# Kernel tuning notes

Measured on AMD Instinct MI355X. Metric: run time of the kernel, lower is better.

## Reference

```python
import jax, jax.numpy as jnp
import numpy as np

N, E, G = 20000, 320000, 256      # nodes, edges, graphs per batch
IN, D, P = 128, 256, 16           # input_dim, out_dim, n_prot
EPS, R, TEMP = 1e-7, 0.5, 0.2


def setup_inputs() -> dict:
    key = jax.random.key(0)
    ks = jax.random.split(key, 9)
    x = jax.random.normal(ks[0], (N, IN), jnp.float32)
    edge_index = jax.random.randint(ks[1], (2, E), 0, N)
    batch = jnp.sort(jax.random.randint(ks[2], (N,), 0, G))
    def w(k, sh):
        fan_in = sh[0]
        return jax.random.normal(k, sh, jnp.float32) * (1.0 / fan_in) ** 0.5
    return {
        "x": x, "edge_index": edge_index, "batch": batch,
        "W1": w(ks[3], (IN, D)), "b1": jnp.zeros((D,), jnp.float32),
        "W2": w(ks[4], (D, D)), "b2": jnp.zeros((D,), jnp.float32),
        "Wm1": w(ks[5], (2 * D, D)), "bm1": jnp.zeros((D,), jnp.float32),
        "Wm2": w(ks[6], (D, 1)), "bm2": jnp.zeros((1,), jnp.float32),
        "prototypes": jax.random.normal(ks[7], (P, D), jnp.float32),
    }


def _cosine(a, b):
    # prototype_distances: cosine similarity with zero-norm -> eps fixup (eval path, no softmax)
    na = jnp.linalg.norm(a, axis=1)
    na = jnp.where(na == 0, na + EPS, na)
    nb = jnp.linalg.norm(b, axis=1)
    nb = jnp.where(nb == 0, nb + EPS, nb)
    return jnp.einsum('ik,jk->ij', a, b) / (na[:, None] * nb[None, :])


def _encoder(x, src, dst, batch, W1, b1, W2, b2, atten=None):
    # 2-layer GIN: h' = relu((h + sum_{j->i} atten_ji * h_j) W + b); graph emb = sum pool
    def conv(h, W, b):
        msg = h[src]                                   # [E, d]
        if atten is not None:
            msg = msg * atten                          # [E, 1] broadcast
        agg = h + jax.ops.segment_sum(msg, dst, num_segments=N)
        return jax.nn.relu(agg @ W + b)
    h = conv(x, W1, b1)
    h = conv(h, W2, b2)
    g = jax.ops.segment_sum(h, batch, num_segments=G)  # [G, D]
    return g, h


def reference(x, edge_index, batch, W1, b1, W2, b2, Wm1, bm1, Wm2, bm2, prototypes):
    src, dst = edge_index[0], edge_index[1]
    graph_embs, node_embs = _encoder(x, src, dst, batch, W1, b1, W2, b2)

    # eval path: assign each graph to nearest prototype by cosine similarity
    sim0 = _cosine(graph_embs, prototypes)             # [G, P]
    assign_prot = jnp.argmax(sim0, axis=1)             # [G]

    # sample_subgraph (eval: plain sigmoid, no gumbel noise)
    node_proto = prototypes[assign_prot[batch]]        # [N, D]
    h = jnp.concatenate([node_embs, node_proto], axis=-1)
    node_prob = jax.nn.relu(h @ Wm1 + bm1) @ Wm2 + bm2  # [N, 1]
    node_bern = jax.nn.sigmoid(node_prob)              # [N, 1]
    edge_bern = node_bern[src] * node_bern[dst]        # [E, 1]

    x2 = x * node_bern
    subgraph_embs, _ = _encoder(x2, src, dst, batch, W1, b1, W2, b2, atten=edge_bern)

    similarity = _cosine(subgraph_embs, prototypes)    # [G, P]

    # NCE loss
    a2 = jnp.argmax(similarity, axis=1)
    onehot = jax.nn.one_hot(a2, P, dtype=similarity.dtype)
    se = jnp.exp(similarity / TEMP)
    pos = (se * onehot).sum(axis=1)
    neg = (se * (1.0 - onehot)).sum(axis=1)
    NCE_loss = -jnp.log(pos / neg).mean()

    # KL regularizers
    nb = node_bern
    KL_node = (nb * jnp.log(nb / R + EPS)
               + (1 - nb) * jnp.log((1 - nb) / (1 - R + EPS) + EPS)).mean()
    eb = edge_bern
    KL_edge = (eb * jnp.log(eb / (R * R) + EPS)
               + (1 - eb) * jnp.log((1 - eb) / (1 - R * R + EPS) + EPS)).mean()
    KL_loss = KL_node + KL_edge

    data_sim = _cosine(subgraph_embs, subgraph_embs)   # [G, G]
    return (KL_loss, NCE_loss, similarity, node_bern, edge_bern,
            data_sim, subgraph_embs, node_embs)
```

## Files before the change

kernel.cpp:

```cpp
#include <hip/hip_runtime.h>
#include <cmath>
#include <cstdint>

#define DINL __device__ __forceinline__

namespace {

constexpr int Nn = 20000, Ee = 320000, Gg = 256, Dd = 256, Pp = 16;
constexpr int Npad = 20096;
constexpr float EPSf = 1e-7f, Rf = 0.5f, TEMPf = 0.2f;

typedef unsigned short u16;
typedef __attribute__((ext_vector_type(8))) short short8;
typedef __attribute__((ext_vector_type(4))) float floatx4;
typedef __attribute__((ext_vector_type(2))) unsigned int u2v;
typedef __attribute__((ext_vector_type(4))) unsigned int u4v;

DINL float waveSum(float x) {
#pragma unroll
  for (int off = 32; off > 0; off >>= 1) x += __shfl_xor(x, off, 64);
  return x;
}

DINL u16 f2bf(float f) {
  unsigned u = __float_as_uint(f);
  unsigned r = u + 0x7fffu + ((u >> 16) & 1u);
  return (u16)(r >> 16);
}
DINL float bf2f(u16 h) { return __uint_as_float(((unsigned)h) << 16); }

__global__ void k_deg(const int* __restrict__ dst, int* __restrict__ deg) {
  int e = blockIdx.x * 256 + threadIdx.x;
  if (e < Ee) atomicAdd(&deg[dst[e]], 1);
}

__global__ __launch_bounds__(1024) void k_pre(const int* __restrict__ deg,
                                              int* __restrict__ offs,
                                              const int* __restrict__ batch,
                                              int* __restrict__ goff) {
  int tid = threadIdx.x;
  if (blockIdx.x == 0) {
    __shared__ int part[1024];
    const int chunk = (Nn + 1023) >> 10;
    int start = tid * chunk;
    int s = 0;
    for (int k = 0; k < chunk; k++) { int i = start + k; if (i < Nn) s += deg[i]; }
    part[tid] = s;
    __syncthreads();
    for (int off = 1; off < 1024; off <<= 1) {
      int v = (tid >= off) ? part[tid - off] : 0;
      __syncthreads();
      part[tid] += v;
      __syncthreads();
    }
    int run = (tid == 0) ? 0 : part[tid - 1];
    for (int k = 0; k < chunk; k++) {
      int i = start + k;
      if (i < Nn) { offs[i] = run; run += deg[i]; }
    }
    if (start < Nn && start + chunk >= Nn) offs[Nn] = run;
  } else {
    for (int i = tid; i < Nn; i += 1024) {
      int bi = batch[i];
      int bp = (i == 0) ? -1 : batch[i - 1];
      for (int g = bp + 1; g <= bi; ++g) goff[g] = i;
      if (i == Nn - 1)
        for (int g = bi + 1; g <= Gg; ++g) goff[g] = Nn;
    }
  }
}

__global__ void k_fill(const int* __restrict__ src, const int* __restrict__ dst,
                       const int* __restrict__ offs, int* __restrict__ cursor,
                       int* __restrict__ csr) {
  int e = blockIdx.x * 256 + threadIdx.x;
  if (e < Ee) {
    int d = dst[e];
    int pos = atomicAdd(&cursor[d], 1);
    csr[offs[d] + pos] = src[e];
  }
}

template <int DIM, int EPL, bool INBF>
DINL void slice(float r[EPL], const void* __restrict__ hv, int row, int ce) {
  if constexpr (INBF) {
    const u16* p = (const u16*)hv + (size_t)row * DIM + ce;
    ushort4 u = *(const ushort4*)p;
    r[0] = bf2f(u.x); r[1] = bf2f(u.y); r[2] = bf2f(u.z); r[3] = bf2f(u.w);
  } else {
    const float* p = (const float*)hv + (size_t)row * DIM + ce;
    float2 u = *(const float2*)p;
    r[0] = u.x; r[1] = u.y;
  }
}

template <int DIM, int MODE, bool INBF, bool OSPL>
__global__ __launch_bounds__(256) void k_aggc(
    const void* __restrict__ hv, const float* __restrict__ nb,
    const int* __restrict__ offs, const int* __restrict__ csr,
    u16* __restrict__ oh, u16* __restrict__ ol) {
  constexpr int EPL = INBF ? 4 : 2;
  constexpr int COLS = EPL * 16;
  constexpr int CHUNKS = DIM / COLS;
  int c = (int)(blockIdx.x % CHUNKS);
  int grp = (int)(blockIdx.x / CHUNKS);
  int wv = threadIdx.x >> 6, lane = threadIdx.x & 63;
  int sub = lane >> 4, l = lane & 15;
  int node = grp * 16 + wv * 4 + sub;
  if (node >= Nn) return;
  int ce = c * COLS + l * EPL;
  float self[EPL], ts[EPL];
  slice<DIM, EPL, INBF>(self, hv, node, ce);
#pragma unroll
  for (int j = 0; j < EPL; j++) ts[j] = 0.f;
  int beg = offs[node], end = offs[node + 1];
  int k = beg;
  for (; k + 4 <= end; k += 4) {
    int s0 = csr[k], s1 = csr[k + 1], s2 = csr[k + 2], s3 = csr[k + 3];
    float r0[EPL], r1[EPL], r2[EPL], r3[EPL];
    slice<DIM, EPL, INBF>(r0, hv, s0, ce);
    slice<DIM, EPL, INBF>(r1, hv, s1, ce);
    slice<DIM, EPL, INBF>(r2, hv, s2, ce);
    slice<DIM, EPL, INBF>(r3, hv, s3, ce);
    if (MODE == 0) {
#pragma unroll
      for (int j = 0; j < EPL; j++) ts[j] += (r0[j] + r1[j]) + (r2[j] + r3[j]);
    } else {
      float w0 = nb[s0], w1 = nb[s1], w2 = nb[s2], w3 = nb[s3];
      if (MODE == 1) { w0 *= w0; w1 *= w1; w2 *= w2; w3 *= w3; }
#pragma unroll
      for (int j = 0; j < EPL; j++)
        ts[j] += (w0 * r0[j] + w1 * r1[j]) + (w2 * r2[j] + w3 * r3[j]);
    }
  }
  for (; k < end; k++) {
    int s = csr[k];
    float r[EPL];
    slice<DIM, EPL, INBF>(r, hv, s, ce);
    if (MODE == 0) {
#pragma unroll
      for (int j = 0; j < EPL; j++) ts[j] += r[j];
    } else {
      float wq = nb[s];
      if (MODE == 1) wq *= wq;
#pragma unroll
      for (int j = 0; j < EPL; j++) ts[j] += wq * r[j];
    }
  }
  float val[EPL];
  if (MODE == 0) {
#pragma unroll
    for (int j = 0; j < EPL; j++) val[j] = self[j] + ts[j];
  } else if (MODE == 1) {
    float wi = nb[node];
#pragma unroll
    for (int j = 0; j < EPL; j++) val[j] = wi * (self[j] + ts[j]);
  } else {
    float wi = nb[node];
#pragma unroll
    for (int j = 0; j < EPL; j++) val[j] = self[j] + wi * ts[j];
  }
  u16 hs[EPL], ls[EPL];
#pragma unroll
  for (int j = 0; j < EPL; j++) {
    hs[j] = f2bf(val[j]);
    if (OSPL) ls[j] = f2bf(val[j] - bf2f(hs[j]));
  }
  u16* po = oh + (size_t)node * DIM + ce;
  if constexpr (EPL == 2) {
    unsigned v = (unsigned)hs[0] | ((unsigned)hs[1] << 16);
    __builtin_nontemporal_store(v, (unsigned*)po);
  } else {
    u2v v;
    v.x = (unsigned)hs[0] | ((unsigned)hs[1] << 16);
    v.y = (unsigned)hs[2] | ((unsigned)hs[3] << 16);
    __builtin_nontemporal_store(v, (u2v*)po);
  }
  if constexpr (OSPL) {
    u16* pl = ol + (size_t)node * DIM + ce;
    if constexpr (EPL == 2) {
      unsigned v = (unsigned)ls[0] | ((unsigned)ls[1] << 16);
      __builtin_nontemporal_store(v, (unsigned*)pl);
    } else {
      u2v v;
      v.x = (unsigned)ls[0] | ((unsigned)ls[1] << 16);
      v.y = (unsigned)ls[2] | ((unsigned)ls[3] << 16);
      __builtin_nontemporal_store(v, (u2v*)pl);
    }
  }
}

template <int K, bool SPLIT, int MODE>
__global__ __launch_bounds__(256) void k_mm(
    const u16* __restrict__ Ah, const u16* __restrict__ Al,
    const u16* __restrict__ Bh, const u16* __restrict__ Bl,
    const float* __restrict__ bias,
    float* __restrict__ outF, u16* __restrict__ outH, u16* __restrict__ outL,
    const float* __restrict__ pc, const int* __restrict__ batch,
    const int* __restrict__ assign, const float* __restrict__ Wm2,
    float* __restrict__ prob) {
  int b = (int)blockIdx.x;
  int g = b >> 5, lane5 = b & 31;
  int panel = g * 8 + (lane5 & 7);
  int col = lane5 >> 3;
  if (panel >= 157) return;
  int rowBase = panel * 128, colBase = col * 64;

  constexpr int SK = 40;
  __shared__ u16 AsH[128 * SK];
  __shared__ u16 AsL[SPLIT ? 128 * SK : 16];
  __shared__ u16 BsH[64 * SK];
  __shared__ u16 BsL[SPLIT ? 64 * SK : 16];
  __shared__ int ap_s[128];
  int t = threadIdx.x;
  if (MODE == 1 && t < 128) {
    int r = rowBase + t;
    ap_s[t] = (r < Nn) ? assign[batch[r]] : 0;
  }
  int lane = t & 63, wv = t >> 6;
  int quad = lane >> 4, l16 = lane & 15;
  int wm = wv * 32;
  floatx4 acc[2][4];
#pragma unroll
  for (int mt = 0; mt < 2; mt++)
#pragma unroll
    for (int nt = 0; nt < 4; nt++) acc[mt][nt] = (floatx4){0.f, 0.f, 0.f, 0.f};

  int ar = t >> 1;
  int ak = (t & 1) * 16;
  const u16* agH = Ah + (size_t)(rowBase + ar) * K + ak;
  const u16* agL = Al + (size_t)(rowBase + ar) * K + ak;
  int bn = t >> 2;
  int bk = (t & 3) * 8;
  const u16* bgH = Bh + (size_t)(colBase + bn) * K + bk;
  const u16* bgL = Bl + (size_t)(colBase + bn) * K + bk;

  u4v cA0 = *(const u4v*)(agH);
  u4v cA1 = *(const u4v*)(agH + 8);
  u4v cB0 = *(const u4v*)(bgH);
  u4v cA0l, cA1l, cB0l;
  if constexpr (SPLIT) {
    cA0l = *(const u4v*)(agL);
    cA1l = *(const u4v*)(agL + 8);
    cB0l = *(const u4v*)(bgL);
  }

  for (int k0 = 0; k0 < K; k0 += 32) {
    __syncthreads();
    *(u4v*)&AsH[ar * SK + ak] = cA0;
    *(u4v*)&AsH[ar * SK + ak + 8] = cA1;
    *(u4v*)&BsH[bn * SK + bk] = cB0;
    if constexpr (SPLIT) {
      *(u4v*)&AsL[ar * SK + ak] = cA0l;
      *(u4v*)&AsL[ar * SK + ak + 8] = cA1l;
      *(u4v*)&BsL[bn * SK + bk] = cB0l;
    }
    __syncthreads();
    if (k0 + 32 < K) {
      cA0 = *(const u4v*)(agH + k0 + 32);
      cA1 = *(const u4v*)(agH + k0 + 40);
      cB0 = *(const u4v*)(bgH + k0 + 32);
      if constexpr (SPLIT) {
        cA0l = *(const u4v*)(agL + k0 + 32);
        cA1l = *(const u4v*)(agL + k0 + 40);
        cB0l = *(const u4v*)(bgL + k0 + 32);
      }
    }
    short8 aH[2], aL[2], bH[4], bL[4];
#pragma unroll
    for (int mt = 0; mt < 2; mt++) {
      int aoff = (wm + mt * 16 + l16) * SK + quad * 8;
      aH[mt] = *(const short8*)&AsH[aoff];
      if (SPLIT) aL[mt] = *(const short8*)&AsL[aoff];
    }
#pragma unroll
    for (int nt = 0; nt < 4; nt++) {
      int boff = (nt * 16 + l16) * SK + quad * 8;
      bH[nt] = *(const short8*)&BsH[boff];
      if (SPLIT) bL[nt] = *(const short8*)&BsL[boff];
    }
#pragma unroll
    for (int mt = 0; mt < 2; mt++)
#pragma unroll
      for (int nt = 0; nt < 4; nt++) {
        acc[mt][nt] = __builtin_amdgcn_mfma_f32_16x16x32_bf16(aH[mt], bH[nt], acc[mt][nt], 0, 0, 0);
        if constexpr (SPLIT) {
          acc[mt][nt] = __builtin_amdgcn_mfma_f32_16x16x32_bf16(aH[mt], bL[nt], acc[mt][nt], 0, 0, 0);
          acc[mt][nt] = __builtin_amdgcn_mfma_f32_16x16x32_bf16(aL[mt], bH[nt], acc[mt][nt], 0, 0, 0);
        }
      }
  }

  if constexpr (MODE == 0) {
#pragma unroll
    for (int mt = 0; mt < 2; mt++)
#pragma unroll
      for (int nt = 0; nt < 4; nt++) {
        int cc = colBase + nt * 16 + l16;
        float bv = bias[cc];
#pragma unroll
        for (int r = 0; r < 4; r++) {
          int row = rowBase + wm + mt * 16 + quad * 4 + r;
          if (row < Nn) {
            float v = fmaxf(acc[mt][nt][r] + bv, 0.f);
            size_t o = (size_t)row * 256 + cc;
            if (outF) outF[o] = v;
            if (outH) {
              u16 hh = f2bf(v);
              outH[o] = hh;
              if (outL) outL[o] = f2bf(v - bf2f(hh));
            }
          }
        }
      }
  } else {
#pragma unroll
    for (int mt = 0; mt < 2; mt++) {
      float part[4] = {0.f, 0.f, 0.f, 0.f};
#pragma unroll
      for (int nt = 0; nt < 4; nt++) {
        int cc = colBase + nt * 16 + l16;
        float wmv = Wm2[cc];
#pragma unroll
        for (int r = 0; r < 4; r++) {
          int ap = ap_s[wm + mt * 16 + quad * 4 + r];
          float tv = fmaxf(acc[mt][nt][r] + pc[ap * 256 + cc], 0.f);
          part[r] += tv * wmv;
        }
      }
#pragma unroll
      for (int r = 0; r < 4; r++) {
#pragma unroll
        for (int off = 1; off < 16; off <<= 1) part[r] += __shfl_xor(part[r], off, 64);
        if (l16 == 0) {
          int row = rowBase + wm + mt * 16 + quad * 4 + r;
          if (row < Nn) atomicAdd(&prob[row], part[r]);
        }
      }
    }
  }
}

__global__ __launch_bounds__(256) void k_poolassign(
    const float* __restrict__ h, const int* __restrict__ goff,
    const float* __restrict__ proto, const float* __restrict__ pnorm,
    int* __restrict__ assign) {
  __shared__ float row[Dd];
  int g = blockIdx.x, c = threadIdx.x;
  int beg = goff[g], end = goff[g + 1];
  float s = 0.f;
  for (int n = beg; n < end; ++n)
    s += __builtin_nontemporal_load(&h[(size_t)n * Dd + c]);
  row[c] = s;
  __syncthreads();
  if (c < 64) {
    float4 v = ((const float4*)row)[c];
    float na = sqrtf(waveSum(v.x * v.x + v.y * v.y + v.z * v.z + v.w * v.w));
    if (na == 0.f) na = EPSf;
    float best = -1e30f;
    int bi = 0;
#pragma unroll
    for (int p = 0; p < Pp; p++) {
      float4 w = *(const float4*)(proto + (size_t)p * Dd + c * 4);
      float d = waveSum(v.x * w.x + v.y * w.y + v.z * w.z + v.w * w.w);
      float sim = d / (na * pnorm[p]);
      if (sim > best) { best = sim; bi = p; }
    }
    if (c == 0) assign[g] = bi;
  }
}

__global__ __launch_bounds__(256) void k_poolsim(
    const float* __restrict__ h, const int* __restrict__ goff,
    const float* __restrict__ proto, const float* __restrict__ pnorm,
    float* __restrict__ o_sg, float* __restrict__ sgemb,
    float* __restrict__ osim, float* __restrict__ snorm,
    float* __restrict__ nceAcc) {
  __shared__ float row[Dd];
  int g = blockIdx.x, c = threadIdx.x;
  int beg = goff[g], end = goff[g + 1];
  float s = 0.f;
  for (int n = beg; n < end; ++n)
    s += __builtin_nontemporal_load(&h[(size_t)n * Dd + c]);
  row[c] = s;
  o_sg[(size_t)g * Dd + c] = s;
  sgemb[(size_t)g * Dd + c] = s;
  __syncthreads();
  if (c < 64) {
    float4 v = ((const float4*)row)[c];
    float na = sqrtf(waveSum(v.x * v.x + v.y * v.y + v.z * v.z + v.w * v.w));
    if (na == 0.f) na = EPSf;
    float sims[Pp];
#pragma unroll
    for (int p = 0; p < Pp; p++) {
      float4 w = *(const float4*)(proto + (size_t)p * Dd + c * 4);
      float d = waveSum(v.x * w.x + v.y * w.y + v.z * w.z + v.w * w.w);
      float sim = d / (na * pnorm[p]);
      sims[p] = sim;
      if (c == p) osim[g * Pp + p] = sim;
    }
    float best = sims[0];
    int bi = 0;
#pragma unroll
    for (int p = 1; p < Pp; p++) {
      if (sims[p] > best) { best = sims[p]; bi = p; }
    }
    float pos = 0.f, neg = 0.f;
#pragma unroll
    for (int p = 0; p < Pp; p++) {
      float e = expf(sims[p] / TEMPf);
      if (p == bi) pos = e; else neg += e;
    }
    if (c == 0) {
      atomicAdd(nceAcc, -logf(pos / neg));
      snorm[g] = na;
    }
  }
}

__global__ void k_berneb(const float* __restrict__ prob, const float* __restrict__ bm2,
                         const int* __restrict__ src, const int* __restrict__ dst,
                         const float* __restrict__ x, u16* __restrict__ xbf,
                         float* __restrict__ ob, float* __restrict__ oe,
                         float* __restrict__ accs) {
  const int nB = (Nn + 255) / 256, eB = (Ee + 255) / 256;
  int b = blockIdx.x;
  if (b < nB) {
    int i = b * 256 + threadIdx.x;
    float val = 0.f;
    if (i < Nn) {
      float z = prob[i] + bm2[0];
      float p = 1.f / (1.f + expf(-z));
      ob[i] = p;
      const float invA = 1.f / Rf, invB = 1.f / (1.f - Rf + EPSf);
      val = p * logf(p * invA + EPSf) + (1.f - p) * logf((1.f - p) * invB + EPSf);
    }
    val = waveSum(val);
    __shared__ float wsum[4];
    int lane = threadIdx.x & 63, wvv = threadIdx.x >> 6;
    if (lane == 0) wsum[wvv] = val;
    __syncthreads();
    if (threadIdx.x == 0) atomicAdd(accs, wsum[0] + wsum[1] + wsum[2] + wsum[3]);
  } else if (b < nB + eB) {
    int e = (b - nB) * 256 + threadIdx.x;
    float val = 0.f;
    if (e < Ee) {
      float zs = prob[src[e]] + bm2[0];
      float zd = prob[dst[e]] + bm2[0];
      float ps = 1.f / (1.f + expf(-zs));
      float pd = 1.f / (1.f + expf(-zd));
      float v = ps * pd;
      __builtin_nontemporal_store(v, &oe[e]);
      const float invA = 1.f / (Rf * Rf), invB = 1.f / (1.f - Rf * Rf + EPSf);
      val = v * logf(v * invA + EPSf) + (1.f - v) * logf((1.f - v) * invB + EPSf);
    }
    val = waveSum(val);
    __shared__ float wsum2[4];
    int lane = threadIdx.x & 63, wvv = threadIdx.x >> 6;
    if (lane == 0) wsum2[wvv] = val;
    __syncthreads();
    if (threadIdx.x == 0) atomicAdd(accs + 1, wsum2[0] + wsum2[1] + wsum2[2] + wsum2[3]);
  } else {
    int i = (b - nB - eB) * 256 + threadIdx.x;
    if (i < Nn * 128 / 4) {
      float4 v = ((const float4*)x)[i];
      u2v o;
      o.x = (unsigned)f2bf(v.x) | ((unsigned)f2bf(v.y) << 16);
      o.y = (unsigned)f2bf(v.z) | ((unsigned)f2bf(v.w) << 16);
      __builtin_nontemporal_store(o, (u2v*)&xbf[(size_t)i * 4]);
    }
  }
}

__global__ void k_datasim(const float* __restrict__ S, const float* __restrict__ snorm,
                          float* __restrict__ out, const float* __restrict__ accs,
                          float* __restrict__ o_kl, float* __restrict__ o_nce) {
  int i = blockIdx.x, j = threadIdx.x;
  if (i == 0 && j == 0) {
    o_kl[0] = accs[0] / (float)Nn + accs[1] / (float)Ee;
    o_nce[0] = accs[2] / (float)Gg;
  }
  __shared__ float si[Dd];
  si[j] = S[(size_t)i * Dd + j];
  __syncthreads();
  const float4* rj = (const float4*)(S + (size_t)j * Dd);
  const float4* sif = (const float4*)si;
  float d = 0.f;
#pragma unroll 4
  for (int k = 0; k < Dd / 4; k++) {
    float4 a = sif[k];
    float4 b = rj[k];
    d += a.x * b.x + a.y * b.y + a.z * b.z + a.w * b.w;
  }
  out[(size_t)i * Gg + j] = d / (snorm[i] * snorm[j]);
}

__global__ void k_prep(const float* __restrict__ W1, const float* __restrict__ W2,
                       const float* __restrict__ Wm1, u16* __restrict__ W1th,
                       u16* __restrict__ W1tl, u16* __restrict__ W2th,
                       u16* __restrict__ W2tl, u16* __restrict__ Wm1th,
                       u16* __restrict__ Wm1tl, const float* __restrict__ proto,
                       const float* __restrict__ bm1, float* __restrict__ pcb,
                       float* __restrict__ pnorm) {
  int blk = blockIdx.x;
  if (blk >= 640) {
    int p = blk - 640, t = threadIdx.x;
    float s = bm1[t];
    for (int k = 0; k < Dd; k++)
      s += proto[p * Dd + k] * Wm1[(size_t)(Dd + k) * Dd + t];
    pcb[p * Dd + t] = s;
    if (t < 64) {
      float4 v = ((const float4*)(proto + (size_t)p * Dd))[t];
      float nsq = waveSum(v.x * v.x + v.y * v.y + v.z * v.z + v.w * v.w);
      if (t == 0) {
        float n = sqrtf(nsq);
        pnorm[p] = (n == 0.f) ? EPSf : n;
      }
    }
    return;
  }
  int idx = blk * 256 + threadIdx.x;
  const float* W;
  u16 *th, *tl;
  int K;
  if (idx < 128 * 256) {
    W = W1; th = W1th; tl = W1tl; K = 128;
  } else if (idx < 128 * 256 + 256 * 256) {
    idx -= 128 * 256;
    W = W2; th = W2th; tl = W2tl; K = 256;
  } else {
    idx -= 128 * 256 + 256 * 256;
    if (idx >= 256 * 256) return;
    W = Wm1; th = Wm1th; tl = Wm1tl; K = 256;
  }
  int k = idx >> 8, n = idx & 255;
  float v = W[idx];
  u16 h = f2bf(v);
  th[(size_t)n * K + k] = h;
  tl[(size_t)n * K + k] = f2bf(v - bf2f(h));
}

}

extern "C" void kernel_launch(void* const* d_in, const int* in_sizes, int n_in,
                              void* d_out, int out_size, void* d_ws, size_t ws_size,
                              hipStream_t stream) {
  const float* x = (const float*)d_in[0];
  const int* ei = (const int*)d_in[1];
  const int* batch = (const int*)d_in[2];
  const float* W1 = (const float*)d_in[3];
  const float* b1 = (const float*)d_in[4];
  const float* W2 = (const float*)d_in[5];
  const float* b2 = (const float*)d_in[6];
  const float* Wm1 = (const float*)d_in[7];
  const float* bm1 = (const float*)d_in[8];
  const float* Wm2 = (const float*)d_in[9];
  const float* bm2 = (const float*)d_in[10];
  const float* proto = (const float*)d_in[11];
  const int* src = ei;
  const int* dst = ei + Ee;

  float* out = (float*)d_out;
  float* o_kl = out;
  float* o_nce = out + 1;
  float* o_sim = out + 2;
  float* o_nb = o_sim + Gg * Pp;
  float* o_eb = o_nb + Nn;
  float* o_ds = o_eb + Ee;
  float* o_sg = o_ds + Gg * Gg;
  float* o_ne = o_sg + Gg * Dd;

  char* w = (char*)d_ws;
  auto take = [&](size_t bytes) -> char* {
    char* p = w;
    w += (bytes + 255) & ~(size_t)255;
    return p;
  };
  const size_t halfR = (size_t)Npad * 256 * 2;
  float* bufB = (float*)take((size_t)Npad * 256 * 4);
  char* R2 = take(2 * halfR);
  u16* A1h = (u16*)R2;
  u16* A1l = (u16*)(R2 + (size_t)Npad * 128 * 2);
  u16* A2h = (u16*)R2;
  u16* A2l = (u16*)(R2 + halfR);
  u16* h1b = (u16*)R2;
  u16* a2bh = (u16*)(R2 + halfR);
  char* R3 = take(2 * halfR);
  u16* neh = (u16*)R3;
  u16* nel = (u16*)(R3 + halfR);
  u16* a1bh = (u16*)R3;
  u16* xbf = (u16*)(R3 + halfR);

  int* csr = (int*)take((size_t)Ee * 4);
  int* deg = (int*)take((size_t)Nn * 4);
  int* cursor = (int*)take((size_t)Nn * 4);
  float* prob = (float*)take(Nn * 4);
  float* accs = (float*)take(16);
  int* offs = (int*)take((size_t)(Nn + 1) * 4);
  int* goff = (int*)take((size_t)(Gg + 1) * 4);
  float* sgemb = (float*)take((size_t)Gg * Dd * 4);
  float* pcb = (float*)take((size_t)Pp * Dd * 4);
  float* pnorm = (float*)take(Pp * 4);
  int* assign = (int*)take(Gg * 4);
  float* snorm = (float*)take(Gg * 4);
  u16* W1th = (u16*)take((size_t)256 * 128 * 2);
  u16* W1tl = (u16*)take((size_t)256 * 128 * 2);
  u16* W2th = (u16*)take((size_t)256 * 256 * 2);
  u16* W2tl = (u16*)take((size_t)256 * 256 * 2);
  u16* Wm1th = (u16*)take((size_t)256 * 256 * 2);
  u16* Wm1tl = (u16*)take((size_t)256 * 256 * 2);

  hipMemsetAsync(deg, 0, 3 * 80128 + 256, stream);

  const int eB = (Ee + 255) / 256;
  const int nB = (Nn + 255) / 256;
  const int gmm = 640;

  k_deg<<<eB, 256, 0, stream>>>(dst, deg);
  k_pre<<<2, 1024, 0, stream>>>(deg, offs, batch, goff);
  k_fill<<<eB, 256, 0, stream>>>(src, dst, offs, cursor, csr);
  k_prep<<<656, 256, 0, stream>>>(W1, W2, Wm1, W1th, W1tl, W2th, W2tl, Wm1th, Wm1tl,
                                  proto, bm1, pcb, pnorm);

  k_aggc<128, 0, false, true><<<1250 * 4, 256, 0, stream>>>(x, nullptr, offs, csr, A1h, A1l);
  k_mm<128, true, 0><<<gmm, 256, 0, stream>>>(A1h, A1l, W1th, W1tl, b1, bufB, nullptr,
                                              nullptr, nullptr, nullptr, nullptr,
                                              nullptr, nullptr);
  k_aggc<256, 0, false, true><<<1250 * 8, 256, 0, stream>>>(bufB, nullptr, offs, csr, A2h, A2l);
  k_mm<256, true, 0><<<gmm, 256, 0, stream>>>(A2h, A2l, W2th, W2tl, b2, o_ne, neh, nel,
                                              nullptr, nullptr, nullptr, nullptr,
                                              nullptr);
  k_poolassign<<<Gg, 256, 0, stream>>>(o_ne, goff, proto, pnorm, assign);
  k_mm<256, true, 1><<<gmm, 256, 0, stream>>>(neh, nel, Wm1th, Wm1tl, nullptr, nullptr,
                                              nullptr, nullptr, pcb, batch, assign,
                                              Wm2, prob);
  k_berneb<<<nB + eB + (Nn * 128 / 4 + 255) / 256, 256, 0, stream>>>(
      prob, bm2, src, dst, x, xbf, o_nb, o_eb, accs);

  k_aggc<128, 1, true, false><<<1250 * 2, 256, 0, stream>>>(xbf, o_nb, offs, csr, a1bh, nullptr);
  k_mm<128, false, 0><<<gmm, 256, 0, stream>>>(a1bh, nullptr, W1th, nullptr, b1, nullptr,
                                               h1b, nullptr, nullptr, nullptr, nullptr,
                                               nullptr, nullptr);
  k_aggc<256, 2, true, false><<<1250 * 4, 256, 0, stream>>>(h1b, o_nb, offs, csr, a2bh, nullptr);
  k_mm<256, false, 0><<<gmm, 256, 0, stream>>>(a2bh, nullptr, W2th, nullptr, b2, bufB,
                                               nullptr, nullptr, nullptr, nullptr,
                                               nullptr, nullptr, nullptr);
  k_poolsim<<<Gg, 256, 0, stream>>>(bufB, goff, proto, pnorm, o_sg, sgemb, o_sim, snorm,
                                    accs + 2);
  k_datasim<<<Gg, 256, 0, stream>>>(sgemb, snorm, o_ds, accs, o_kl, o_nce);
}
```

Measured before the change: 438.6 us.

## Fuse setup kernels, fold graph pooling into GEMM epilogue, read fp32 A directly

Merges the degree count, weight transpose/split, prototype prep, x-to-bf16 conversion and graph offset computation into one setup kernel, which removes several launches. The final GEMM's epilogue now accumulates sum-pooled subgraph embeddings with atomics, so the full node-embedding buffer is no longer written and re-read by the pooling kernel. The MLP GEMM now loads fp32 node embeddings and splits them into bf16 hi/lo on the fly, so the separate hi/lo copies are no longer stored. Atomic contention on 256x256 pooled rows and extra conversion work inside the GEMM loop are the tradeoffs, and the atomic float sums make the output order-dependent.

```diff
diff --git a/kernel.cpp b/kernel.cpp
--- a/kernel.cpp
+++ b/kernel.cpp
@@ -29,38 +29,66 @@
 }
 DINL float bf2f(u16 h) { return __uint_as_float(((unsigned)h) << 16); }
 
-__global__ void k_deg(const int* __restrict__ dst, int* __restrict__ deg) {
-  int e = blockIdx.x * 256 + threadIdx.x;
-  if (e < Ee) atomicAdd(&deg[dst[e]], 1);
-}
-
-__global__ __launch_bounds__(1024) void k_pre(const int* __restrict__ deg,
-                                              int* __restrict__ offs,
-                                              const int* __restrict__ batch,
-                                              int* __restrict__ goff) {
+__global__ void k_setup(const int* __restrict__ dst, int* __restrict__ deg,
+                        const float* __restrict__ W1, const float* __restrict__ W2,
+                        const float* __restrict__ Wm1, u16* __restrict__ W1th,
+                        u16* __restrict__ W1tl, u16* __restrict__ W2th,
+                        u16* __restrict__ W2tl, u16* __restrict__ Wm1th,
+                        u16* __restrict__ Wm1tl, const float* __restrict__ proto,
+                        const float* __restrict__ bm1, float* __restrict__ pcb,
+                        float* __restrict__ pnorm, const float* __restrict__ x,
+                        u16* __restrict__ xbf, const int* __restrict__ batch,
+                        int* __restrict__ goff) {
+  const int eB = (Ee + 255) / 256;
+  int blk = blockIdx.x;
   int tid = threadIdx.x;
-  if (blockIdx.x == 0) {
-    __shared__ int part[1024];
-    const int chunk = (Nn + 1023) >> 10;
-    int start = tid * chunk;
-    int s = 0;
-    for (int k = 0; k < chunk; k++) { int i = start + k; if (i < Nn) s += deg[i]; }
-    part[tid] = s;
-    __syncthreads();
-    for (int off = 1; off < 1024; off <<= 1) {
-      int v = (tid >= off) ? part[tid - off] : 0;
-      __syncthreads();
-      part[tid] += v;
-      __syncthreads();
-    }
-    int run = (tid == 0) ? 0 : part[tid - 1];
-    for (int k = 0; k < chunk; k++) {
-      int i = start + k;
-      if (i < Nn) { offs[i] = run; run += deg[i]; }
-    }
-    if (start < Nn && start + chunk >= Nn) offs[Nn] = run;
-  } else {
-    for (int i = tid; i < Nn; i += 1024) {
+  if (blk < eB) {
+    int e = blk * 256 + tid;
+    if (e < Ee) atomicAdd(&deg[dst[e]], 1);
+  } else if (blk < eB + 640) {
+    int idx = (blk - eB) * 256 + tid;
+    const float* W;
+    u16 *th, *tl;
+    int K;
+    if (idx < 128 * 256) {
+      W = W1; th = W1th; tl = W1tl; K = 128;
+    } else if (idx < 128 * 256 + 256 * 256) {
+      idx -= 128 * 256;
+      W = W2; th = W2th; tl = W2tl; K = 256;
+    } else {
+      idx -= 128 * 256 + 256 * 256;
+      W = Wm1; th = Wm1th; tl = Wm1tl; K = 256;
+    }
+    int k = idx >> 8, n = idx & 255;
+    float v = W[idx];
+    u16 h = f2bf(v);
+    th[(size_t)n * K + k] = h;
+    tl[(size_t)n * K + k] = f2bf(v - bf2f(h));
+  } else if (blk < eB + 656) {
+    int p = blk - eB - 640;
+    float s = bm1[tid];
+    for (int k = 0; k < Dd; k++)
+      s += proto[p * Dd + k] * Wm1[(size_t)(Dd + k) * Dd + tid];
+    pcb[p * Dd + tid] = s;
+    if (tid < 64) {
+      float4 v = ((const float4*)(proto + (size_t)p * Dd))[tid];
+      float nsq = waveSum(v.x * v.x + v.y * v.y + v.z * v.z + v.w * v.w);
+      if (tid == 0) {
+        float n = sqrtf(nsq);
+        pnorm[p] = (n == 0.f) ? EPSf : n;
+      }
+    }
+  } else if (blk < eB + 656 + 2500) {
+    int i = (blk - eB - 656) * 256 + tid;
+    if (i < Nn * 128 / 4) {
+      float4 v = ((const float4*)x)[i];
+      u2v o;
+      o.x = (unsigned)f2bf(v.x) | ((unsigned)f2bf(v.y) << 16);
+      o.y = (unsigned)f2bf(v.z) | ((unsigned)f2bf(v.w) << 16);
+      __builtin_nontemporal_store(o, (u2v*)&xbf[(size_t)i * 4]);
+    }
+  } else {
+    for (int i = tid; i < Nn; i += 256) {
       int bi = batch[i];
       int bp = (i == 0) ? -1 : batch[i - 1];
       for (int g = bp + 1; g <= bi; ++g) goff[g] = i;
@@ -68,6 +96,30 @@
         for (int g = bi + 1; g <= Gg; ++g) goff[g] = Nn;
     }
   }
+}
+
+__global__ __launch_bounds__(1024) void k_scan(const int* __restrict__ deg,
+                                               int* __restrict__ offs) {
+  __shared__ int part[1024];
+  int tid = threadIdx.x;
+  const int chunk = (Nn + 1023) >> 10;
+  int start = tid * chunk;
+  int s = 0;
+  for (int k = 0; k < chunk; k++) { int i = start + k; if (i < Nn) s += deg[i]; }
+  part[tid] = s;
+  __syncthreads();
+  for (int off = 1; off < 1024; off <<= 1) {
+    int v = (tid >= off) ? part[tid - off] : 0;
+    __syncthreads();
+    part[tid] += v;
+    __syncthreads();
+  }
+  int run = (tid == 0) ? 0 : part[tid - 1];
+  for (int k = 0; k < chunk; k++) {
+    int i = start + k;
+    if (i < Nn) { offs[i] = run; run += deg[i]; }
+  }
+  if (start < Nn && start + chunk >= Nn) offs[Nn] = run;
 }
 
 __global__ void k_fill(const int* __restrict__ src, const int* __restrict__ dst,
@@ -190,15 +242,15 @@
   }
 }
 
-template <int K, bool SPLIT, int MODE>
+template <int K, bool SPLIT, bool AF32, int EPI>
 __global__ __launch_bounds__(256) void k_mm(
-    const u16* __restrict__ Ah, const u16* __restrict__ Al,
+    const void* __restrict__ Av, const u16* __restrict__ Al,
     const u16* __restrict__ Bh, const u16* __restrict__ Bl,
     const float* __restrict__ bias,
-    float* __restrict__ outF, u16* __restrict__ outH, u16* __restrict__ outL,
+    float* __restrict__ outF, u16* __restrict__ outH,
     const float* __restrict__ pc, const int* __restrict__ batch,
     const int* __restrict__ assign, const float* __restrict__ Wm2,
-    float* __restrict__ prob) {
+    float* __restrict__ prob, float* __restrict__ sgemb) {
   int b = (int)blockIdx.x;
   int g = b >> 5, lane5 = b & 31;
   int panel = g * 8 + (lane5 & 7);
@@ -213,9 +265,10 @@
   __shared__ u16 BsL[SPLIT ? 64 * SK : 16];
   __shared__ int ap_s[128];
   int t = threadIdx.x;
-  if (MODE == 1 && t < 128) {
+  if ((EPI == 2 || EPI == 3) && t < 128) {
     int r = rowBase + t;
-    ap_s[t] = (r < Nn) ? assign[batch[r]] : 0;
+    int bv = (r < Nn) ? batch[r] : 0;
+    ap_s[t] = (EPI == 2) ? ((r < Nn) ? assign[bv] : 0) : bv;
   }
   int lane = t & 63, wv = t >> 6;
   int quad = lane >> 4, l16 = lane & 15;
@@ -228,43 +281,84 @@
 
   int ar = t >> 1;
   int ak = (t & 1) * 16;
-  const u16* agH = Ah + (size_t)(rowBase + ar) * K + ak;
-  const u16* agL = Al + (size_t)(rowBase + ar) * K + ak;
   int bn = t >> 2;
   int bk = (t & 3) * 8;
   const u16* bgH = Bh + (size_t)(colBase + bn) * K + bk;
   const u16* bgL = Bl + (size_t)(colBase + bn) * K + bk;
 
-  u4v cA0 = *(const u4v*)(agH);
-  u4v cA1 = *(const u4v*)(agH + 8);
-  u4v cB0 = *(const u4v*)(bgH);
-  u4v cA0l, cA1l, cB0l;
-  if constexpr (SPLIT) {
-    cA0l = *(const u4v*)(agL);
-    cA1l = *(const u4v*)(agL + 8);
-    cB0l = *(const u4v*)(bgL);
-  }
+  const u16* agH;
+  const u16* agL;
+  const float* agF;
+  if constexpr (AF32) {
+    agF = (const float*)Av + (size_t)(rowBase + ar) * K + ak;
+  } else {
+    agH = (const u16*)Av + (size_t)(rowBase + ar) * K + ak;
+    agL = Al + (size_t)(rowBase + ar) * K + ak;
+  }
+  bool aok = AF32 ? (rowBase + ar < Nn) : true;
+
+  u4v cA0, cA1, cA0l, cA1l, cB0, cB0l;
+  float4 fA[4];
+  if constexpr (AF32) {
+#pragma unroll
+    for (int q = 0; q < 4; q++)
+      fA[q] = aok ? ((const float4*)agF)[q] : make_float4(0.f, 0.f, 0.f, 0.f);
+  } else {
+    cA0 = *(const u4v*)(agH);
+    cA1 = *(const u4v*)(agH + 8);
+    if constexpr (SPLIT) {
+      cA0l = *(const u4v*)(agL);
+      cA1l = *(const u4v*)(agL + 8);
+    }
+  }
+  cB0 = *(const u4v*)(bgH);
+  if constexpr (SPLIT) cB0l = *(const u4v*)(bgL);
 
   for (int k0 = 0; k0 < K; k0 += 32) {
     __syncthreads();
-    *(u4v*)&AsH[ar * SK + ak] = cA0;
-    *(u4v*)&AsH[ar * SK + ak + 8] = cA1;
+    if constexpr (AF32) {
+      u16 hh[16], ll[16];
+#pragma unroll
+      for (int q = 0; q < 4; q++) {
+        const float vv[4] = {fA[q].x, fA[q].y, fA[q].z, fA[q].w};
+#pragma unroll
+        for (int j = 0; j < 4; j++) {
+          u16 h = f2bf(vv[j]);
+          hh[q * 4 + j] = h;
+          ll[q * 4 + j] = f2bf(vv[j] - bf2f(h));
+        }
+      }
+      *(u4v*)&AsH[ar * SK + ak] = *(const u4v*)&hh[0];
+      *(u4v*)&AsH[ar * SK + ak + 8] = *(const u4v*)&hh[8];
+      *(u4v*)&AsL[ar * SK + ak] = *(const u4v*)&ll[0];
+      *(u4v*)&AsL[ar * SK + ak + 8] = *(const u4v*)&ll[8];
+    } else {
+      *(u4v*)&AsH[ar * SK + ak] = cA0;
+      *(u4v*)&AsH[ar * SK + ak + 8] = cA1;
+      if constexpr (SPLIT) {
+        *(u4v*)&AsL[ar * SK + ak] = cA0l;
+        *(u4v*)&AsL[ar * SK + ak + 8] = cA1l;
+      }
+    }
     *(u4v*)&BsH[bn * SK + bk] = cB0;
-    if constexpr (SPLIT) {
-      *(u4v*)&AsL[ar * SK + ak] = cA0l;
-      *(u4v*)&AsL[ar * SK + ak + 8] = cA1l;
-      *(u4v*)&BsL[bn * SK + bk] = cB0l;
-    }
+    if constexpr (SPLIT) *(u4v*)&BsL[bn * SK + bk] = cB0l;
     __syncthreads();
     if (k0 + 32 < K) {
-      cA0 = *(const u4v*)(agH + k0 + 32);
-      cA1 = *(const u4v*)(agH + k0 + 40);
+      if constexpr (AF32) {
+#pragma unroll
+        for (int q = 0; q < 4; q++)
+          fA[q] = aok ? ((const float4*)(agF + k0 + 32))[q]
+                      : make_float4(0.f, 0.f, 0.f, 0.f);
+      } else {
+        cA0 = *(const u4v*)(agH + k0 + 32);
+        cA1 = *(const u4v*)(agH + k0 + 40);
+        if constexpr (SPLIT) {
+          cA0l = *(const u4v*)(agL + k0 + 32);
+          cA1l = *(const u4v*)(agL + k0 + 40);
+        }
+      }
       cB0 = *(const u4v*)(bgH + k0 + 32);
-      if constexpr (SPLIT) {
-        cA0l = *(const u4v*)(agL + k0 + 32);
-        cA1l = *(const u4v*)(agL + k0 + 40);
-        cB0l = *(const u4v*)(bgL + k0 + 32);
-      }
+      if constexpr (SPLIT) cB0l = *(const u4v*)(bgL + k0 + 32);
     }
     short8 aH[2], aL[2], bH[4], bL[4];
 #pragma unroll
@@ -291,7 +385,7 @@
       }
   }
 
-  if constexpr (MODE == 0) {
+  if constexpr (EPI == 0 || EPI == 1 || EPI == 3) {
 #pragma unroll
     for (int mt = 0; mt < 2; mt++)
 #pragma unroll
@@ -300,15 +394,16 @@
         float bv = bias[cc];
 #pragma unroll
         for (int r = 0; r < 4; r++) {
-          int row = rowBase + wm + mt * 16 + quad * 4 + r;
+          int lr = wm + mt * 16 + quad * 4 + r;
+          int row = rowBase + lr;
           if (row < Nn) {
             float v = fmaxf(acc[mt][nt][r] + bv, 0.f);
-            size_t o = (size_t)row * 256 + cc;
-            if (outF) outF[o] = v;
-            if (outH) {
-              u16 hh = f2bf(v);
-              outH[o] = hh;
-              if (outL) outL[o] = f2bf(v - bf2f(hh));
+            if constexpr (EPI == 0) {
+              outF[(size_t)row * 256 + cc] = v;
+            } else if constexpr (EPI == 1) {
+              outH[(size_t)row * 256 + cc] = f2bf(v);
+            } else {
+              atomicAdd(&sgemb[(size_t)ap_s[lr] * 256 + cc], v);
             }
           }
         }
@@ -370,21 +465,16 @@
   }
 }
 
-__global__ __launch_bounds__(256) void k_poolsim(
-    const float* __restrict__ h, const int* __restrict__ goff,
-    const float* __restrict__ proto, const float* __restrict__ pnorm,
-    float* __restrict__ o_sg, float* __restrict__ sgemb,
+__global__ __launch_bounds__(256) void k_simfin(
+    const float* __restrict__ sgemb, const float* __restrict__ proto,
+    const float* __restrict__ pnorm, float* __restrict__ o_sg,
     float* __restrict__ osim, float* __restrict__ snorm,
     float* __restrict__ nceAcc) {
   __shared__ float row[Dd];
   int g = blockIdx.x, c = threadIdx.x;
-  int beg = goff[g], end = goff[g + 1];
-  float s = 0.f;
-  for (int n = beg; n < end; ++n)
-    s += __builtin_nontemporal_load(&h[(size_t)n * Dd + c]);
+  float s = sgemb[(size_t)g * Dd + c];
   row[c] = s;
   o_sg[(size_t)g * Dd + c] = s;
-  sgemb[(size_t)g * Dd + c] = s;
   __syncthreads();
   if (c < 64) {
     float4 v = ((const float4*)row)[c];
@@ -420,10 +510,9 @@
 
 __global__ void k_berneb(const float* __restrict__ prob, const float* __restrict__ bm2,
                          const int* __restrict__ src, const int* __restrict__ dst,
-                         const float* __restrict__ x, u16* __restrict__ xbf,
                          float* __restrict__ ob, float* __restrict__ oe,
                          float* __restrict__ accs) {
-  const int nB = (Nn + 255) / 256, eB = (Ee + 255) / 256;
+  const int nB = (Nn + 255) / 256;
   int b = blockIdx.x;
   if (b < nB) {
     int i = b * 256 + threadIdx.x;
@@ -441,7 +530,7 @@
     if (lane == 0) wsum[wvv] = val;
     __syncthreads();
     if (threadIdx.x == 0) atomicAdd(accs, wsum[0] + wsum[1] + wsum[2] + wsum[3]);
-  } else if (b < nB + eB) {
+  } else {
     int e = (b - nB) * 256 + threadIdx.x;
     float val = 0.f;
     if (e < Ee) {
@@ -460,15 +549,6 @@
     if (lane == 0) wsum2[wvv] = val;
     __syncthreads();
     if (threadIdx.x == 0) atomicAdd(accs + 1, wsum2[0] + wsum2[1] + wsum2[2] + wsum2[3]);
-  } else {
-    int i = (b - nB - eB) * 256 + threadIdx.x;
-    if (i < Nn * 128 / 4) {
-      float4 v = ((const float4*)x)[i];
-      u2v o;
-      o.x = (unsigned)f2bf(v.x) | ((unsigned)f2bf(v.y) << 16);
-      o.y = (unsigned)f2bf(v.z) | ((unsigned)f2bf(v.w) << 16);
-      __builtin_nontemporal_store(o, (u2v*)&xbf[(size_t)i * 4]);
-    }
   }
 }
 
@@ -493,51 +573,6 @@
     d += a.x * b.x + a.y * b.y + a.z * b.z + a.w * b.w;
   }
   out[(size_t)i * Gg + j] = d / (snorm[i] * snorm[j]);
-}
-
-__global__ void k_prep(const float* __restrict__ W1, const float* __restrict__ W2,
-                       const float* __restrict__ Wm1, u16* __restrict__ W1th,
-                       u16* __restrict__ W1tl, u16* __restrict__ W2th,
-                       u16* __restrict__ W2tl, u16* __restrict__ Wm1th,
-                       u16* __restrict__ Wm1tl, const float* __restrict__ proto,
-                       const float* __restrict__ bm1, float* __restrict__ pcb,
-                       float* __restrict__ pnorm) {
-  int blk = blockIdx.x;
-  if (blk >= 640) {
-    int p = blk - 640, t = threadIdx.x;
-    float s = bm1[t];
-    for (int k = 0; k < Dd; k++)
-      s += proto[p * Dd + k] * Wm1[(size_t)(Dd + k) * Dd + t];
-    pcb[p * Dd + t] = s;
-    if (t < 64) {
-      float4 v = ((const float4*)(proto + (size_t)p * Dd))[t];
-      float nsq = waveSum(v.x * v.x + v.y * v.y + v.z * v.z + v.w * v.w);
-      if (t == 0) {
-        float n = sqrtf(nsq);
-        pnorm[p] = (n == 0.f) ? EPSf : n;
-      }
-    }
-    return;
-  }
-  int idx = blk * 256 + threadIdx.x;
-  const float* W;
-  u16 *th, *tl;
-  int K;
-  if (idx < 128 * 256) {
-    W = W1; th = W1th; tl = W1tl; K = 128;
-  } else if (idx < 128 * 256 + 256 * 256) {
-    idx -= 128 * 256;
-    W = W2; th = W2th; tl = W2tl; K = 256;
-  } else {
-    idx -= 128 * 256 + 256 * 256;
-    if (idx >= 256 * 256) return;
-    W = Wm1; th = Wm1th; tl = Wm1tl; K = 256;
-  }
-  int k = idx >> 8, n = idx & 255;
-  float v = W[idx];
-  u16 h = f2bf(v);
-  th[(size_t)n * K + k] = h;
-  tl[(size_t)n * K + k] = f2bf(v - bf2f(h));
 }
 
 }
@@ -585,20 +620,17 @@
   u16* A2l = (u16*)(R2 + halfR);
   u16* h1b = (u16*)R2;
   u16* a2bh = (u16*)(R2 + halfR);
-  char* R3 = take(2 * halfR);
-  u16* neh = (u16*)R3;
-  u16* nel = (u16*)(R3 + halfR);
-  u16* a1bh = (u16*)R3;
-  u16* xbf = (u16*)(R3 + halfR);
+  u16* a1bh = (u16*)take((size_t)Npad * 128 * 2);
+  u16* xbf = (u16*)take((size_t)Nn * 128 * 2);
 
   int* csr = (int*)take((size_t)Ee * 4);
   int* deg = (int*)take((size_t)Nn * 4);
   int* cursor = (int*)take((size_t)Nn * 4);
   float* prob = (float*)take(Nn * 4);
   float* accs = (float*)take(16);
+  float* sgemb = (float*)take((size_t)Gg * Dd * 4);
   int* offs = (int*)take((size_t)(Nn + 1) * 4);
   int* goff = (int*)take((size_t)(Gg + 1) * 4);
-  float* sgemb = (float*)take((size_t)Gg * Dd * 4);
   float* pcb = (float*)take((size_t)Pp * Dd * 4);
   float* pnorm = (float*)take(Pp * 4);
   int* assign = (int*)take(Gg * 4);
@@ -610,42 +642,40 @@
   u16* Wm1th = (u16*)take((size_t)256 * 256 * 2);
   u16* Wm1tl = (u16*)take((size_t)256 * 256 * 2);
 
-  hipMemsetAsync(deg, 0, 3 * 80128 + 256, stream);
+  hipMemsetAsync(deg, 0, 3 * 80128 + 256 + (size_t)Gg * Dd * 4, stream);
 
   const int eB = (Ee + 255) / 256;
   const int nB = (Nn + 255) / 256;
   const int gmm = 640;
 
-  k_deg<<<eB, 256, 0, stream>>>(dst, deg);
-  k_pre<<<2, 1024, 0, stream>>>(deg, offs, batch, goff);
+  k_setup<<<eB + 656 + 2500 + 1, 256, 0, stream>>>(
+      dst, deg, W1, W2, Wm1, W1th, W1tl, W2th, W2tl, Wm1th, Wm1tl, proto, bm1,
+      pcb, pnorm, x, xbf, batch, goff);
+  k_scan<<<1, 1024, 0, stream>>>(deg, offs);
   k_fill<<<eB, 256, 0, stream>>>(src, dst, offs, cursor, csr);
-  k_prep<<<656, 256, 0, stream>>>(W1, W2, Wm1, W1th, W1tl, W2th, W2tl, Wm1th, Wm1tl,
-                                  proto, bm1, pcb, pnorm);
 
   k_aggc<128, 0, false, true><<<1250 * 4, 256, 0, stream>>>(x, nullptr, offs, csr, A1h, A1l);
-  k_mm<128, true, 0><<<gmm, 256, 0, stream>>>(A1h, A1l, W1th, W1tl, b1, bufB, nullptr,
-                                              nullptr, nullptr, nullptr, nullptr,
-                                              nullptr, nullptr);
+  k_mm<128, true, false, 0><<<gmm, 256, 0, stream>>>(A1h, A1l, W1th, W1tl, b1, bufB,
+                                                     nullptr, nullptr, nullptr, nullptr,
+                                                     nullptr, nullptr, nullptr);
   k_aggc<256, 0, false, true><<<1250 * 8, 256, 0, stream>>>(bufB, nullptr, offs, csr, A2h, A2l);
-  k_mm<256, true, 0><<<gmm, 256, 0, stream>>>(A2h, A2l, W2th, W2tl, b2, o_ne, neh, nel,
-                                              nullptr, nullptr, nullptr, nullptr,
-                                              nullptr);
+  k_mm<256, true, false, 0><<<gmm, 256, 0, stream>>>(A2h, A2l, W2th, W2tl, b2, o_ne,
+                                                     nullptr, nullptr, nullptr, nullptr,
+                                                     nullptr, nullptr, nullptr);
   k_poolassign<<<Gg, 256, 0, stream>>>(o_ne, goff, proto, pnorm, assign);
-  k_mm<256, true, 1><<<gmm, 256, 0, stream>>>(neh, nel, Wm1th, Wm1tl, nullptr, nullptr,
-                                              nullptr, nullptr, pcb, batch, assign,
-                                              Wm2, prob);
-  k_berneb<<<nB + eB + (Nn * 128 / 4 + 255) / 256, 256, 0, stream>>>(
-      prob, bm2, src, dst, x, xbf, o_nb, o_eb, accs);
+  k_mm<256, true, true, 2><<<gmm, 256, 0, stream>>>(o_ne, nullptr, Wm1th, Wm1tl,
+                                                    nullptr, nullptr, nullptr, pcb,
+                                                    batch, assign, Wm2, prob, nullptr);
+  k_berneb<<<nB + eB, 256, 0, stream>>>(prob, bm2, src, dst, o_nb, o_eb, accs);
 
   k_aggc<128, 1, true, false><<<1250 * 2, 256, 0, stream>>>(xbf, o_nb, offs, csr, a1bh, nullptr);
-  k_mm<128, false, 0><<<gmm, 256, 0, stream>>>(a1bh, nullptr, W1th, nullptr, b1, nullptr,
-                                               h1b, nullptr, nullptr, nullptr, nullptr,
-                                               nullptr, nullptr);
+  k_mm<128, false, false, 1><<<gmm, 256, 0, stream>>>(a1bh, nullptr, W1th, nullptr, b1,
+                                                      nullptr, h1b, nullptr, nullptr,
+                                                      nullptr, nullptr, nullptr, nullptr);
   k_aggc<256, 2, true, false><<<1250 * 4, 256, 0, stream>>>(h1b, o_nb, offs, csr, a2bh, nullptr);
-  k_mm<256, false, 0><<<gmm, 256, 0, stream>>>(a2bh, nullptr, W2th, nullptr, b2, bufB,
-                                               nullptr, nullptr, nullptr, nullptr,
-                                               nullptr, nullptr, nullptr);
-  k_poolsim<<<Gg, 256, 0, stream>>>(bufB, goff, proto, pnorm, o_sg, sgemb, o_sim, snorm,
-                                    accs + 2);
+  k_mm<256, false, false, 3><<<gmm, 256, 0, stream>>>(a2bh, nullptr, W2th, nullptr, b2,
+                                                      nullptr, nullptr, nullptr, batch,
+                                                      nullptr, nullptr, nullptr, sgemb);
+  k_simfin<<<Gg, 256, 0, stream>>>(sgemb, proto, pnorm, o_sg, o_sim, snorm, accs + 2);
   k_datasim<<<Gg, 256, 0, stream>>>(sgemb, snorm, o_ds, accs, o_kl, o_nce);
 }
```

Result: slower. 490.1 us (+11.7%).
